# Optimization experiments

Hardware: AMD Instinct MI355X
Metric: run time of the kernel (lower is better)

The kernel has to match this reference:

```python
import jax, jax.numpy as jnp
import numpy as np

MAX_STEPS = 5  # forward calls plan_geodesic_path(max_steps=5)


def setup_inputs() -> dict:
    key = jax.random.key(0)
    k1, k2, k3 = jax.random.split(key, 3)
    B, D, L = 8192, 1024, 4096
    x = jax.random.normal(k1, (B, D), dtype=jnp.float32)
    target = jax.random.normal(k2, (B, D), dtype=jnp.float32)
    landmarks = jax.random.normal(k3, (L, D), dtype=jnp.float32)  # nn.Parameter init torch.randn
    adjacency = jnp.eye(L, dtype=bool)  # nn.Parameter(torch.eye(L)) > 0, non-trainable
    return {"x": x, "target": target, "landmarks": landmarks, "adjacency": adjacency}


def _nearest_landmark(pts, landmarks):
    # argmin of squared euclidean distance == argmin of cdist
    d2 = (jnp.sum(pts * pts, axis=-1, keepdims=True)
          - 2.0 * pts @ landmarks.T
          + jnp.sum(landmarks * landmarks, axis=-1)[None, :])  # [B, L]
    return jnp.argmin(d2, axis=-1)


def _forward(x, target, landmarks, adjacency):
    eps = 1e-7
    start_idx = _nearest_landmark(x, landmarks)       # [B]
    end_idx = _nearest_landmark(target, landmarks)    # [B]
    # geodesic distance between all landmark pairs: arccos of cosine similarity
    ln = landmarks / jnp.linalg.norm(landmarks, axis=-1, keepdims=True)
    cos = jnp.clip(ln @ ln.T, -1.0 + eps, 1.0 - eps)  # [L, L]
    geo = jnp.arccos(cos)
    # dist_to_end[b, l] = geodesic dist from landmark l to the end landmark of sample b
    dist_to_end = geo[end_idx]                        # [B, L] (geo symmetric)

    def step(cur, _):
        mask = adjacency[cur]                         # [B, L] neighbor mask
        d = jnp.where(mask, dist_to_end, jnp.inf)
        best = jnp.argmin(d, axis=-1)                 # greedy neighbor closest to end
        done = cur == end_idx
        new = jnp.where(done, end_idx, best)          # once at end, stay at end
        return new, landmarks[new]                    # path coord at this step

    _, coords = jax.lax.scan(step, start_idx, None, length=MAX_STEPS - 1)
    # coords: [MAX_STEPS-1, B, D]; path = [x, coords...]; output = path[:, -1]
    return coords[-1]


def reference(x, target, landmarks, adjacency):
    return _forward(x, target, landmarks, adjacency)
```

## Files before the change

kernel.cpp:

```cpp
#include <hip/hip_runtime.h>
#include <math.h>


typedef unsigned short u16;
typedef unsigned int u32;
typedef unsigned long long u64;
typedef __attribute__((ext_vector_type(4))) int i32x4;

constexpr int Bn = 8192, Dn = 1024, Ln = 4096;
constexpr int NCB = Ln / 256;
constexpr int KCAND = 8;
constexpr int MARGIN_Q = 8192;
constexpr int NXBLK = Bn * Dn / 16 / 256;

__device__ __forceinline__ void gload16(const void* g, void* s) {
    __builtin_amdgcn_global_load_lds((const __attribute__((address_space(1))) void*)g,
                                     (__attribute__((address_space(3))) void*)s, 16, 0, 0);
}

__global__ __launch_bounds__(256) void prep_kernel(
    const float* __restrict__ x, const float* __restrict__ lm,
    char* __restrict__ xq, char* __restrict__ lq,
    float* __restrict__ lmsq, int* __restrict__ lmsq_q)
{
    int bid = blockIdx.x;
    if (bid < NXBLK) {
        int i = bid * 256 + threadIdx.x;
        const float4* s4 = (const float4*)(x + (size_t)i * 16);
        u32 w[4];
        #pragma unroll
        for (int k = 0; k < 4; ++k) {
            float4 v = s4[k];
            int q0 = __float2int_rn(v.x * 24.f), q1 = __float2int_rn(v.y * 24.f);
            int q2 = __float2int_rn(v.z * 24.f), q3 = __float2int_rn(v.w * 24.f);
            q0 = min(127, max(-127, q0)); q1 = min(127, max(-127, q1));
            q2 = min(127, max(-127, q2)); q3 = min(127, max(-127, q3));
            w[k] = (u32)(q0 & 255) | ((u32)(q1 & 255) << 8)
                 | ((u32)(q2 & 255) << 16) | ((u32)(q3 & 255) << 24);
        }
        i32x4 o = { (int)w[0], (int)w[1], (int)w[2], (int)w[3] };
        *(i32x4*)(xq + (size_t)i * 16) = o;
    } else {
        int l = bid - NXBLK;
        int t = threadIdx.x;
        float4 v = *(const float4*)(lm + (size_t)l * Dn + t * 4);
        float s = v.x * v.x + v.y * v.y + v.z * v.z + v.w * v.w;
        int q0 = __float2int_rn(v.x * 24.f), q1 = __float2int_rn(v.y * 24.f);
        int q2 = __float2int_rn(v.z * 24.f), q3 = __float2int_rn(v.w * 24.f);
        q0 = min(127, max(-127, q0)); q1 = min(127, max(-127, q1));
        q2 = min(127, max(-127, q2)); q3 = min(127, max(-127, q3));
        int sq = q0 * q0 + q1 * q1 + q2 * q2 + q3 * q3;
        u32 packed = (u32)(q0 & 255) | ((u32)(q1 & 255) << 8)
                   | ((u32)(q2 & 255) << 16) | ((u32)(q3 & 255) << 24);
        *(u32*)(lq + (size_t)l * Dn + t * 4) = packed;
        #pragma unroll
        for (int off = 32; off > 0; off >>= 1) {
            s += __shfl_down(s, off);
            sq += __shfl_down(sq, off);
        }
        __shared__ float redf[4];
        __shared__ int redi[4];
        if ((t & 63) == 0) { redf[t >> 6] = s; redi[t >> 6] = sq; }
        __syncthreads();
        if (t == 0) {
            lmsq[l] = redf[0] + redf[1] + redf[2] + redf[3];
            lmsq_q[l] = redi[0] + redi[1] + redi[2] + redi[3];
        }
    }
}

struct Epi {
    int wm_s[128][4];
    int wm_i[128][4];
    int bmin_s[128];
    u32 cnt_s[128];
    u16 cand_s[128][KCAND];
    int csc_s[128][KCAND];
};

__global__ __launch_bounds__(512, 4) void score_kernel(
    const char* __restrict__ xq, const char* __restrict__ lq,
    const int* __restrict__ lmsq_q,
    int* __restrict__ bws_min, u32* __restrict__ bws_cnt,
    u16* __restrict__ bws_cand, int* __restrict__ bws_csc)
{
    __shared__ char LDSM[73728];
    char* As = LDSM;
    char* Bs = LDSM + 24576;

    const int tid = threadIdx.x;
    const int lane = tid & 63, w = tid >> 6;
    const int wm = w >> 2, wn = w & 3;
    const int l15 = lane & 15, lhi = lane >> 4;

    const u32 bid = blockIdx.y * gridDim.x + blockIdx.x;
    const u32 xcd = bid & 7, i2 = bid >> 3;
    const long brow = (long)(xcd * 8 + (i2 & 7)) * 128;
    const long bcol = (long)(i2 >> 3) * 256;

    i32x4 accT[4][4];
    #pragma unroll
    for (int j = 0; j < 4; ++j)
        #pragma unroll
        for (int q = 0; q < 4; ++q) accT[j][q] = (i32x4)0;

    const int rowA = tid >> 2, c4A = tid & 3;
    const int rowB1 = 128 + (tid >> 2);
    const char* gA  = xq + (brow + rowA) * (long)Dn + (c4A ^ ((rowA >> 1) & 3)) * 16;
    const char* gB0 = lq + (bcol + rowA) * (long)Dn + (c4A ^ ((rowA >> 1) & 3)) * 16;
    const char* gB1 = lq + (bcol + rowB1) * (long)Dn + (c4A ^ ((rowB1 >> 1) & 3)) * 16;
    const int aw = w * 1024;

    const int slot = lhi ^ ((l15 >> 1) & 3);
    const char* ldsA = As + (wm * 64 + l15) * 64 + slot * 16;
    const char* ldsB = Bs + (wn * 64 + l15) * 64 + slot * 16;

    i32x4 aa[4], bb[4];

#define STAGE(IDX) do {                                                    \
        gload16(gA,  As + (IDX) * 8192 + aw);                              \
        gload16(gB0, Bs + (IDX) * 16384 + aw);                             \
        gload16(gB1, Bs + (IDX) * 16384 + 8192 + aw);                      \
        gA += 64; gB0 += 64; gB1 += 64; } while (0)

#define STEP(CUR, STG, VM) do {                                            \
        STG;                                                               \
        _Pragma("unroll")                                                  \
        for (int i = 0; i < 4; ++i)                                        \
            aa[i] = *(const i32x4*)(ldsA + (CUR) * 8192 + i * 1024);       \
        _Pragma("unroll")                                                  \
        for (int j = 0; j < 4; ++j)                                        \
            bb[j] = *(const i32x4*)(ldsB + (CUR) * 16384 + j * 1024);      \
        __builtin_amdgcn_s_setprio(1);                                     \
        _Pragma("unroll")                                                  \
        for (int j = 0; j < 4; ++j)                                        \
            _Pragma("unroll")                                              \
            for (int i = 0; i < 4; ++i)                                    \
                accT[j][i] = __builtin_amdgcn_mfma_i32_16x16x64_i8(        \
                    bb[j], aa[i], accT[j][i], 0, 0, 0);                    \
        __builtin_amdgcn_s_setprio(0);                                     \
        asm volatile("s_waitcnt lgkmcnt(0)" ::: "memory");                 \
        asm volatile("s_waitcnt vmcnt(" #VM ")" ::: "memory");             \
        __builtin_amdgcn_sched_barrier(0);                                 \
        __builtin_amdgcn_s_barrier(); } while (0)

    STAGE(0); STAGE(1);
    asm volatile("s_waitcnt vmcnt(3)" ::: "memory");
    __builtin_amdgcn_s_barrier();

    #pragma unroll 1
    for (int u = 0; u < 4; ++u) {
        STEP(0, STAGE(2), 3);
        STEP(1, STAGE(0), 3);
        STEP(2, STAGE(1), 3);
    }
    STEP(0, STAGE(2), 3);
    STEP(1, STAGE(0), 3);
    STEP(2, {}, 0);
    STEP(0, {}, 0);

    __syncthreads();

    Epi* e = (Epi*)LDSM;
    if (tid < 128) e->cnt_s[tid] = 0;

    int sqq[4][4];
    #pragma unroll
    for (int j = 0; j < 4; ++j)
        #pragma unroll
        for (int r = 0; r < 4; ++r)
            sqq[j][r] = lmsq_q[bcol + wn * 64 + j * 16 + lhi * 4 + r];
    __syncthreads();

    #pragma unroll
    for (int q = 0; q < 4; ++q) {
        int bs = 0x7fffffff; int bi = 0x7fffffff;
        #pragma unroll
        for (int j = 0; j < 4; ++j)
            #pragma unroll
            for (int r = 0; r < 4; ++r) {
                int s = sqq[j][r] - 2 * accT[j][q][r];
                int idx = wn * 64 + j * 16 + lhi * 4 + r;
                if (s < bs || (s == bs && idx < bi)) { bs = s; bi = idx; }
            }
        #pragma unroll
        for (int m = 16; m < 64; m <<= 1) {
            int os = __shfl_xor(bs, m);
            int oi = __shfl_xor(bi, m);
            if (os < bs || (os == bs && oi < bi)) { bs = os; bi = oi; }
        }
        if (lhi == 0) {
            int row = wm * 64 + q * 16 + l15;
            e->wm_s[row][wn] = bs; e->wm_i[row][wn] = bi;
        }
    }
    __syncthreads();
    if (tid < 128) {
        int bs = 0x7fffffff; int bi = 0x7fffffff;
        #pragma unroll
        for (int c = 0; c < 4; ++c) {
            int s = e->wm_s[tid][c]; int i3 = e->wm_i[tid][c];
            if (s < bs || (s == bs && i3 < bi)) { bs = s; bi = i3; }
        }
        e->bmin_s[tid] = bs;
    }
    __syncthreads();
    #pragma unroll
    for (int q = 0; q < 4; ++q) {
        int row = wm * 64 + q * 16 + l15;
        int thr = e->bmin_s[row] + MARGIN_Q;
        #pragma unroll
        for (int j = 0; j < 4; ++j)
            #pragma unroll
            for (int r = 0; r < 4; ++r) {
                int s = sqq[j][r] - 2 * accT[j][q][r];
                if (s <= thr) {
                    u32 p = atomicAdd(&e->cnt_s[row], 1u);
                    if (p < KCAND) {
                        e->cand_s[row][p] = (u16)(bcol + wn * 64 + j * 16 + lhi * 4 + r);
                        e->csc_s[row][p] = s;
                    }
                }
            }
    }
    __syncthreads();
    if (tid < 128) {
        long g = (brow + tid) * NCB + (bcol >> 8);
        bws_min[g] = e->bmin_s[tid];
        bws_cnt[g] = e->cnt_s[tid];
        #pragma unroll
        for (int p = 0; p < KCAND; ++p) bws_cand[g * KCAND + p] = e->cand_s[tid][p];
        #pragma unroll
        for (int p = 0; p < KCAND; ++p) bws_csc[g * KCAND + p] = e->csc_s[tid][p];
    }
}

__device__ __forceinline__ void eval_cand(int ci, const float4 xr[4],
                                          const float* __restrict__ lm,
                                          const float* __restrict__ lmsq,
                                          int lane, float& best_s, int& best_i) {
    float d = 0.f;
    #pragma unroll
    for (int q = 0; q < 4; ++q) {
        float4 lv = *(const float4*)(lm + (size_t)ci * Dn + (q * 64 + lane) * 4);
        d += xr[q].x * lv.x + xr[q].y * lv.y + xr[q].z * lv.z + xr[q].w * lv.w;
    }
    #pragma unroll
    for (int m = 1; m < 64; m <<= 1) d += __shfl_xor(d, m);
    float s = lmsq[ci] - 2.f * d;
    if (s < best_s || (s == best_s && ci < best_i)) { best_s = s; best_i = ci; }
}

__global__ __launch_bounds__(256) void merge_kernel(
    const float* __restrict__ x, const float* __restrict__ lm,
    const float* __restrict__ lmsq,
    const int* __restrict__ bws_min, const u32* __restrict__ bws_cnt,
    const u16* __restrict__ bws_cand, const int* __restrict__ bws_csc,
    float* __restrict__ out)
{
    const int b = blockIdx.x * 4 + (threadIdx.x >> 6);
    const int lane = threadIdx.x & 63;
    const size_t gb = (size_t)b * NCB;

    int v = (lane < NCB) ? bws_min[gb + lane] : 0x7fffffff;
    int vm = v;
    #pragma unroll
    for (int m = 1; m < 64; m <<= 1) vm = min(vm, __shfl_xor(vm, m));
    const int thr = vm + MARGIN_Q;
    const u64 mask = __ballot(lane < NCB && v <= thr);

    int ncand = 0, uniq = 0;
    u64 m0 = mask;
    while (m0) {
        int nb = (int)__ffsll(m0) - 1; m0 &= m0 - 1;
        u32 c = bws_cnt[gb + nb];
        if (c > KCAND) { ncand += 1000; continue; }
        int sc = (lane < (int)c) ? bws_csc[(gb + nb) * KCAND + lane] : 0x7fffffff;
        u64 pm = __ballot(sc <= thr);
        ncand += (int)__popcll(pm);
        if (pm) uniq = bws_cand[(gb + nb) * KCAND + ((int)__ffsll(pm) - 1)];
    }

    int best_i;
    if (ncand == 1) {
        best_i = uniq;
    } else {
        float4 xr[4];
        #pragma unroll
        for (int q = 0; q < 4; ++q)
            xr[q] = *(const float4*)(x + (size_t)b * Dn + (q * 64 + lane) * 4);
        float best_s = INFINITY; best_i = 0x7fffffff;
        m0 = mask;
        while (m0) {
            int nb = (int)__ffsll(m0) - 1; m0 &= m0 - 1;
            u32 c = bws_cnt[gb + nb];
            if (c <= KCAND) {
                for (u32 p = 0; p < c; ++p) {
                    if (bws_csc[(gb + nb) * KCAND + p] > thr) continue;
                    int ci = bws_cand[(gb + nb) * KCAND + p];
                    eval_cand(ci, xr, lm, lmsq, lane, best_s, best_i);
                }
            } else {
                for (int col = 0; col < 256; ++col)
                    eval_cand(nb * 256 + col, xr, lm, lmsq, lane, best_s, best_i);
            }
        }
    }
    #pragma unroll
    for (int q = 0; q < 4; ++q)
        *(float4*)(out + (size_t)b * Dn + (q * 64 + lane) * 4) =
            *(const float4*)(lm + (size_t)best_i * Dn + (q * 64 + lane) * 4);
}

extern "C" void kernel_launch(void* const* d_in, const int* in_sizes, int n_in,
                              void* d_out, int out_size, void* d_ws, size_t ws_size,
                              hipStream_t stream) {
    const float* x   = (const float*)d_in[0];
    const float* lmf = (const float*)d_in[2];
    float* out = (float*)d_out;

    char* xq = (char*)d_ws;
    char* lq = xq + (size_t)Bn * Dn;
    float* lmsq = (float*)(lq + (size_t)Ln * Dn);
    int* lmsqq = (int*)(lmsq + Ln);
    int* bws_min = lmsqq + Ln;
    u32* bws_cnt = (u32*)(bws_min + (size_t)Bn * NCB);
    u16* bws_cand = (u16*)(bws_cnt + (size_t)Bn * NCB);
    int* bws_csc = (int*)(bws_cand + (size_t)Bn * NCB * KCAND);

    prep_kernel<<<NXBLK + Ln, 256, 0, stream>>>(x, lmf, xq, lq, lmsq, lmsqq);
    dim3 g(64, 16);
    score_kernel<<<g, 512, 0, stream>>>(xq, lq, lmsqq, bws_min, bws_cnt, bws_cand, bws_csc);
    merge_kernel<<<Bn / 4, 256, 0, stream>>>(x, lmf, lmsq, bws_min, bws_cnt, bws_cand, bws_csc, out);
}
```

Before: 86.17 us.

## Load A operand straight into registers with double buffering, stage only B in LDS

The int8 GEMM score kernel now reads the x (A) tiles from global memory directly into a pair of register buffers that alternate each step, and keeps only the landmark (B) tiles in a three-slot LDS ring filled by global_load_lds. This shrinks the LDS footprint and drops the LDS reads for A. In exchange, each wave fetches its A rows from global memory on its own, so rows are loaded several times across waves. The vmcnt(2) wait before each barrier also forces the A loads issued in that step to finish, so their latency is only partly hidden behind the MFMAs. The final prefetch reads one K-chunk past the row end.

```diff
diff --git a/kernel.cpp b/kernel.cpp
--- a/kernel.cpp
+++ b/kernel.cpp
@@ -84,9 +84,8 @@
     int* __restrict__ bws_min, u32* __restrict__ bws_cnt,
     u16* __restrict__ bws_cand, int* __restrict__ bws_csc)
 {
-    __shared__ char LDSM[73728];
-    char* As = LDSM;
-    char* Bs = LDSM + 24576;
+    __shared__ char LDSM[49152];
+    char* Bs = LDSM;
 
     const int tid = threadIdx.x;
     const int lane = tid & 63, w = tid >> 6;
@@ -104,60 +103,69 @@
         #pragma unroll
         for (int q = 0; q < 4; ++q) accT[j][q] = (i32x4)0;
 
-    const int rowA = tid >> 2, c4A = tid & 3;
-    const int rowB1 = 128 + (tid >> 2);
-    const char* gA  = xq + (brow + rowA) * (long)Dn + (c4A ^ ((rowA >> 1) & 3)) * 16;
-    const char* gB0 = lq + (bcol + rowA) * (long)Dn + (c4A ^ ((rowA >> 1) & 3)) * 16;
-    const char* gB1 = lq + (bcol + rowB1) * (long)Dn + (c4A ^ ((rowB1 >> 1) & 3)) * 16;
+    const char* xb_blk = xq + brow * (long)Dn;
+    int va = (wm * 64 + l15) * Dn + lhi * 16;
+
+    const int rowB = tid >> 2, c4B = tid & 3;
+    const int rowB1 = 128 + rowB;
+    const char* gB0 = lq + (bcol + rowB) * (long)Dn + ((c4B ^ ((rowB >> 1) & 3)) * 16);
+    const char* gB1 = lq + (bcol + rowB1) * (long)Dn + ((c4B ^ ((rowB1 >> 1) & 3)) * 16);
     const int aw = w * 1024;
 
     const int slot = lhi ^ ((l15 >> 1) & 3);
-    const char* ldsA = As + (wm * 64 + l15) * 64 + slot * 16;
     const char* ldsB = Bs + (wn * 64 + l15) * 64 + slot * 16;
 
-    i32x4 aa[4], bb[4];
-
-#define STAGE(IDX) do {                                                    \
-        gload16(gA,  As + (IDX) * 8192 + aw);                              \
+    i32x4 aa0[4], aa1[4], bb[4];
+
+#define LOADA(DST) do {                                                    \
+        DST[0] = *(const i32x4*)(xb_blk + va);                             \
+        DST[1] = *(const i32x4*)(xb_blk + va + 16384);                     \
+        DST[2] = *(const i32x4*)(xb_blk + va + 32768);                     \
+        DST[3] = *(const i32x4*)(xb_blk + va + 49152);                     \
+        va += 64; } while (0)
+
+#define STGB(IDX) do {                                                     \
         gload16(gB0, Bs + (IDX) * 16384 + aw);                             \
         gload16(gB1, Bs + (IDX) * 16384 + 8192 + aw);                      \
-        gA += 64; gB0 += 64; gB1 += 64; } while (0)
-
-#define STEP(CUR, STG, VM) do {                                            \
-        STG;                                                               \
-        _Pragma("unroll")                                                  \
-        for (int i = 0; i < 4; ++i)                                        \
-            aa[i] = *(const i32x4*)(ldsA + (CUR) * 8192 + i * 1024);       \
+        gB0 += 64; gB1 += 64; } while (0)
+
+#define STEPD(BCUR, BSTG, AAU, AAL, VM) do {                               \
+        LOADA(AAL);                                                        \
+        STGB(BSTG);                                                        \
         _Pragma("unroll")                                                  \
         for (int j = 0; j < 4; ++j)                                        \
-            bb[j] = *(const i32x4*)(ldsB + (CUR) * 16384 + j * 1024);      \
+            bb[j] = *(const i32x4*)(ldsB + (BCUR) * 16384 + j * 1024);     \
         __builtin_amdgcn_s_setprio(1);                                     \
         _Pragma("unroll")                                                  \
         for (int j = 0; j < 4; ++j)                                        \
             _Pragma("unroll")                                              \
             for (int i = 0; i < 4; ++i)                                    \
                 accT[j][i] = __builtin_amdgcn_mfma_i32_16x16x64_i8(        \
-                    bb[j], aa[i], accT[j][i], 0, 0, 0);                    \
+                    bb[j], AAU[i], accT[j][i], 0, 0, 0);                   \
         __builtin_amdgcn_s_setprio(0);                                     \
         asm volatile("s_waitcnt lgkmcnt(0)" ::: "memory");                 \
         asm volatile("s_waitcnt vmcnt(" #VM ")" ::: "memory");             \
         __builtin_amdgcn_sched_barrier(0);                                 \
         __builtin_amdgcn_s_barrier(); } while (0)
 
-    STAGE(0); STAGE(1);
-    asm volatile("s_waitcnt vmcnt(3)" ::: "memory");
+    LOADA(aa0);
+    STGB(0); STGB(1);
+    asm volatile("s_waitcnt vmcnt(2)" ::: "memory");
     __builtin_amdgcn_s_barrier();
 
     #pragma unroll 1
-    for (int u = 0; u < 4; ++u) {
-        STEP(0, STAGE(2), 3);
-        STEP(1, STAGE(0), 3);
-        STEP(2, STAGE(1), 3);
-    }
-    STEP(0, STAGE(2), 3);
-    STEP(1, STAGE(0), 3);
-    STEP(2, {}, 0);
-    STEP(0, {}, 0);
+    for (int u = 0; u < 2; ++u) {
+        STEPD(0, 2, aa0, aa1, 2);
+        STEPD(1, 0, aa1, aa0, 2);
+        STEPD(2, 1, aa0, aa1, 2);
+        STEPD(0, 2, aa1, aa0, 2);
+        STEPD(1, 0, aa0, aa1, 2);
+        STEPD(2, 1, aa1, aa0, 2);
+    }
+    STEPD(0, 2, aa0, aa1, 2);
+    STEPD(1, 0, aa1, aa0, 2);
+    STEPD(2, 1, aa0, aa1, 2);
+    STEPD(0, 2, aa1, aa0, 0);
 
     __syncthreads();
 
```

After: 130.2 us. 1.51x slower.
